# Kernel tuning notes

Hardware: AMD Instinct MI355X
Metric: run time of the kernel (lower is better)

The kernel has to match this reference:

```python
import jax, jax.numpy as jnp
import numpy as np

A_MAX = 7  # 2**A_bits - 1 with A_bits=3
W_HI = 7   # torch.randint(0, 2**W_bits - 1) -> values in [0, 6]


def _conv_valid(x, w):
    # x: [N,C,H,W] float32, w: [O,I,kh,kw] float32; stride 1, no padding
    return jax.lax.conv_general_dilated(
        x, w, window_strides=(1, 1), padding='VALID',
        dimension_numbers=('NCHW', 'OIHW', 'NCHW'))


def setup_inputs() -> dict:
    key = jax.random.key(0)
    k_x, k_w = jax.random.split(key)
    x = jax.random.randint(k_x, (16, 64, 112, 112), 0, 8, dtype=jnp.int32)
    # 3-bit weights of the original 7x7 conv, values 0..6
    W7 = jax.random.randint(k_w, (128, 64, 7, 7), 0, W_HI).astype(jnp.float32)
    w1 = W7[:, :, :, 0:3]
    w2 = W7[:, :, :, 2:5]
    w2 = w2.at[:, :, :, 0].set(0.0)
    w2 = w2.at[:, :, :, 2].set(0.0)
    w3 = W7[:, :, :, 4:7]
    return {"x": x, "w1": w1, "w2": w2, "w3": w3}


def reference(x, w1, w2, w3):
    # 3-bit activation quantization: clip int input to [0, 7]
    xc = jnp.clip(x, 0, A_MAX).astype(jnp.float32)
    out1 = _conv_valid(xc[:, :, :, :-2], w1)   # [N,O,H-6,W-4]
    out2 = _conv_valid(xc, w2)                 # [N,O,H-6,W-2]
    out3 = _conv_valid(xc[:, :, :, 2:], w3)    # [N,O,H-6,W-4]
    # combine slices -> equivalent to valid 7x7 conv: [N,O,H-6,W-6]
    return out1[:, :, :, :-2] + out2[:, :, :, 2:-2] + out3[:, :, :, 2:]
```

## Files before the change

kernel.cpp:

```cpp
#include <hip/hip_runtime.h>
#include <cstdint>

typedef __attribute__((ext_vector_type(4))) int i32x4;

#define XROWS  22
#define ROWB   2048
#define WSLICE 8192
#define WB_BYTES 409600
#define XT_BYTES ((size_t)16 * 112 * 128 * 64)

__device__ __forceinline__ void g2lds16(const void* g, void* l) {
  __builtin_amdgcn_global_load_lds(
      (const __attribute__((address_space(1))) unsigned int*)g,
      (__attribute__((address_space(3))) unsigned int*)l, 16, 0, 0);
}

__global__ void prep_w(const float* __restrict__ w1,
                       const float* __restrict__ w2,
                       const float* __restrict__ w3,
                       signed char* __restrict__ wb) {
  int t = blockIdx.x * 256 + threadIdx.x;
  int lo = t & 15;
  int co = (t >> 4) & 127;
  int g  = (t >> 11) & 3;
  int s  = t >> 13;
  if (s >= 49) return;
  int kh = s / 7, kw = s % 7;
  int ci = g * 16 + lo;
  int base = ((co * 64 + ci) * 7 + kh) * 3;
  float v;
  if (kw < 3)       v = w1[base + kw];
  else if (kw == 3) v = w2[base + 1];
  else              v = w3[base + kw - 4];
  wb[t] = (signed char)(int)v;
}

__global__ void prep_x(const int* __restrict__ x, signed char* __restrict__ xt) {
  __shared__ unsigned char T[64 * 68];
  const int tid = threadIdx.x;
  const int wt = blockIdx.x * 64, h = blockIdx.y, n = blockIdx.z;
  {
    const int wr = tid & 63;
    const int cb = (tid >> 6) * 16;
    int ws = wt + wr; ws = ws < 112 ? ws : 111;
    const int* xp = x + (((size_t)n * 64 + cb) * 112 + h) * 112 + ws;
    #pragma unroll
    for (int g4 = 0; g4 < 4; ++g4) {
      uint32_t v = 0;
      #pragma unroll
      for (int j = 0; j < 4; ++j) {
        int a = xp[(g4 * 4 + j) * 12544];
        a = a < 0 ? 0 : (a > 7 ? 7 : a);
        v |= (uint32_t)a << (8 * j);
      }
      *(uint32_t*)&T[wr * 68 + cb + g4 * 4] = v;
    }
  }
  __syncthreads();
  {
    const int wo = tid >> 2, q = tid & 3;
    const int key = ((wt + wo) >> 1) & 3;
    const int sg = (q ^ key) << 4;
    int4 v;
    v.x = *(const int*)&T[wo * 68 + sg + 0];
    v.y = *(const int*)&T[wo * 68 + sg + 4];
    v.z = *(const int*)&T[wo * 68 + sg + 8];
    v.w = *(const int*)&T[wo * 68 + sg + 12];
    *(int4*)&xt[(((size_t)n * 112 + h) * 128 + wt + wo) * 64 + q * 16] = v;
  }
}

#define MFMA(acc, a, b) acc = __builtin_amdgcn_mfma_i32_16x16x64_i8(a, b, acc, 0, 0, 0)

template<bool XT>
__global__ __launch_bounds__(256, 3)
void conv7(const int* __restrict__ x, const signed char* __restrict__ xt,
           const signed char* __restrict__ wb, float* __restrict__ out) {
  __shared__ __align__(16) unsigned char Xs[XROWS * ROWB];

  const int tid  = threadIdx.x;
  const int lane = tid & 63;
  const int wid  = tid >> 6;
  const int lrow = lane & 15;
  const int lkg  = lane >> 4;

  const int L  = blockIdx.x;
  const int Lp = (L & 7) * 196 + (L >> 3);
  const int coh = Lp & 1;
  const int r2  = Lp >> 1;
  const int bx  = r2 % 7;
  const int t7  = r2 / 7;
  const int by  = t7 % 7;
  const int n   = t7 / 7;
  const int ho_base = by * 16;
  const int wo_base = bx * 16;

  const signed char* aB = wb + lkg * 2048 + coh * 1024 + lrow * 16;

  i32x4 A[4];
  #pragma unroll
  for (int m = 0; m < 4; ++m) A[m] = *(const i32x4*)(aB + m * 256);

  if constexpr (XT) {
    for (int r = wid; r < XROWS; r += 4) {
      int h = ho_base + r; h = h < 112 ? h : 111;
      const signed char* src = xt + (((size_t)n * 112 + h) * 128 + wo_base) * 64;
      g2lds16(src + lane * 16, &Xs[r * ROWB]);
      g2lds16(src + 1024 + lane * 16, &Xs[r * ROWB + 1024]);
    }
    asm volatile("s_waitcnt vmcnt(0)" ::: "memory");
  } else {
    const int w_a  = tid & 15,       cg_a  = tid >> 4;
    const int w_b2 = 16 + (tid & 7), cg_b2 = tid >> 3;
    const bool doB = (tid < 128) && ((tid & 7) < 6);
    const int keyA = ((w_a >> 1) & 3) << 2;
    const int keyB = ((w_b2 >> 1) & 3) << 2;
    for (int r = 0; r < XROWS; ++r) {
      int h = ho_base + r; h = h < 112 ? h : 111;
      const int* xr = x + (size_t)n * 64 * 12544 + h * 112;
      {
        int wc = wo_base + w_a; wc = wc < 112 ? wc : 111;
        uint32_t v = 0;
        #pragma unroll
        for (int j = 0; j < 4; ++j) {
          int a = xr[(cg_a * 4 + j) * 12544 + wc];
          a = a < 0 ? 0 : (a > 7 ? 7 : a);
          v |= (uint32_t)a << (8 * j);
        }
        *(uint32_t*)&Xs[r * ROWB + w_a * 64 + ((cg_a ^ keyA) << 2)] = v;
      }
      if (doB) {
        int wc = wo_base + w_b2; wc = wc < 112 ? wc : 111;
        uint32_t v = 0;
        #pragma unroll
        for (int j = 0; j < 4; ++j) {
          int a = xr[(cg_b2 * 4 + j) * 12544 + wc];
          a = a < 0 ? 0 : (a > 7 ? 7 : a);
          v |= (uint32_t)a << (8 * j);
        }
        *(uint32_t*)&Xs[r * ROWB + w_b2 * 64 + ((cg_b2 ^ keyB) << 2)] = v;
      }
    }
  }
  __syncthreads();

  i32x4 acc[4][4];
  #pragma unroll
  for (int m = 0; m < 4; ++m)
    #pragma unroll
    for (int b = 0; b < 4; ++b)
      acc[m][b] = (i32x4){0, 0, 0, 0};

  const int rowB = wid * 4;

  for (int kw = 0; kw < 7; ++kw) {
    const int w_l  = lrow + kw;
    const int bcol = w_l * 64 + ((lkg ^ ((w_l >> 1) & 3)) << 4);
    i32x4 B[8];
    #pragma unroll
    for (int b = 0; b < 4; ++b)
      B[b] = *(const i32x4*)&Xs[(rowB + b) * ROWB + bcol];

    #pragma unroll
    for (int kh = 0; kh < 7; ++kh) {
      if (kh < 6)
        B[(kh + 4) & 7] = *(const i32x4*)&Xs[(rowB + kh + 4) * ROWB + bcol];
      const signed char* apn = aB + (size_t)(kh < 6 ? (kh + 1) * 7 + kw : kw + 1) * WSLICE;
      __builtin_amdgcn_s_setprio(1);
      #pragma unroll
      for (int m = 0; m < 4; ++m) {
        #pragma unroll
        for (int b = 0; b < 4; ++b)
          MFMA(acc[m][b], A[m], B[(kh + b) & 7]);
        A[m] = *(const i32x4*)(apn + m * 256);
      }
      __builtin_amdgcn_s_setprio(0);
    }
  }

  const int wo = wo_base + lrow;
  if (wo < 106) {
    #pragma unroll
    for (int m = 0; m < 4; ++m) {
      const int co = coh * 64 + m * 16 + lkg * 4;
      #pragma unroll
      for (int b = 0; b < 4; ++b) {
        const int ho = ho_base + rowB + b;
        if (ho < 106) {
          float* op = out + (((size_t)n * 128 + co) * 106 + ho) * 106 + wo;
          #pragma unroll
          for (int j = 0; j < 4; ++j)
            op[(size_t)j * 11236] = (float)acc[m][b][j];
        }
      }
    }
  }
}

extern "C" void kernel_launch(void* const* d_in, const int* in_sizes, int n_in,
                              void* d_out, int out_size, void* d_ws, size_t ws_size,
                              hipStream_t stream) {
  const int*   x  = (const int*)d_in[0];
  const float* w1 = (const float*)d_in[1];
  const float* w2 = (const float*)d_in[2];
  const float* w3 = (const float*)d_in[3];
  float* outp = (float*)d_out;
  signed char* wbp = (signed char*)d_ws;
  signed char* xtp = wbp + WB_BYTES;

  prep_w<<<dim3(1568), dim3(256), 0, stream>>>(w1, w2, w3, wbp);
  if (ws_size >= WB_BYTES + XT_BYTES) {
    prep_x<<<dim3(2, 112, 16), dim3(256), 0, stream>>>(x, xtp);
    conv7<true><<<dim3(1568), dim3(256), 0, stream>>>(x, xtp, wbp, outp);
  } else {
    conv7<false><<<dim3(1568), dim3(256), 0, stream>>>(x, xtp, wbp, outp);
  }
}
```

Before: 84.38 us.

## Fuse weight prep into x prep and make conv a persistent atomic-queue kernel

Merges the weight-packing kernel into the activation-transpose kernel, which saves one launch and also resets a tile counter in workspace. The main conv becomes persistent: 768 blocks pull tiles from a global atomic counter in a loop instead of launching 1568 one-shot blocks. The goals are lower launch overhead and a better-balanced tail. The cost is an atomic plus a barrier per tile, and losing the L2-friendly XCD-aware tile remapping the old kernel used. The setprio hints are also dropped in the fallback path.

```diff
diff --git a/kernel.cpp b/kernel.cpp
--- a/kernel.cpp
+++ b/kernel.cpp
@@ -7,7 +7,10 @@
 #define ROWB   2048
 #define WSLICE 8192
 #define WB_BYTES 409600
+#define CTR_OFF  401408
 #define XT_BYTES ((size_t)16 * 112 * 128 * 64)
+#define NTILES 1568
+#define PERSIST_BLOCKS 768
 
 __device__ __forceinline__ void g2lds16(const void* g, void* l) {
   __builtin_amdgcn_global_load_lds(
@@ -35,10 +38,36 @@
   wb[t] = (signed char)(int)v;
 }
 
-__global__ void prep_x(const int* __restrict__ x, signed char* __restrict__ xt) {
+__global__ void prep_xw(const int* __restrict__ x,
+                        const float* __restrict__ w1,
+                        const float* __restrict__ w2,
+                        const float* __restrict__ w3,
+                        signed char* __restrict__ xt,
+                        signed char* __restrict__ wb,
+                        unsigned int* __restrict__ ctr) {
   __shared__ unsigned char T[64 * 68];
   const int tid = threadIdx.x;
   const int wt = blockIdx.x * 64, h = blockIdx.y, n = blockIdx.z;
+  const int fid = (blockIdx.z * 112 + blockIdx.y) * 2 + blockIdx.x;
+
+  if (fid == 0 && tid == 0) *ctr = 0;
+
+  if (fid < 1568) {
+    int t = fid * 256 + tid;
+    int lo = t & 15;
+    int co = (t >> 4) & 127;
+    int g  = (t >> 11) & 3;
+    int s  = t >> 13;
+    int kh = s / 7, kw = s % 7;
+    int ci = g * 16 + lo;
+    int base = ((co * 64 + ci) * 7 + kh) * 3;
+    float v;
+    if (kw < 3)       v = w1[base + kw];
+    else if (kw == 3) v = w2[base + 1];
+    else              v = w3[base + kw - 4];
+    wb[t] = (signed char)(int)v;
+  }
+
   {
     const int wr = tid & 63;
     const int cb = (tid >> 6) * 16;
@@ -72,10 +101,105 @@
 
 #define MFMA(acc, a, b) acc = __builtin_amdgcn_mfma_i32_16x16x64_i8(a, b, acc, 0, 0, 0)
 
-template<bool XT>
 __global__ __launch_bounds__(256, 3)
-void conv7(const int* __restrict__ x, const signed char* __restrict__ xt,
-           const signed char* __restrict__ wb, float* __restrict__ out) {
+void conv7p(const signed char* __restrict__ xt,
+            const signed char* __restrict__ wb,
+            float* __restrict__ out,
+            unsigned int* __restrict__ ctr) {
+  __shared__ __align__(16) unsigned char Xs[XROWS * ROWB];
+  __shared__ unsigned int ts;
+
+  const int tid  = threadIdx.x;
+  const int lane = tid & 63;
+  const int wid  = tid >> 6;
+  const int lrow = lane & 15;
+  const int lkg  = lane >> 4;
+  const int rowB = wid * 4;
+
+  for (;;) {
+    if (tid == 0) ts = atomicAdd(ctr, 1u);
+    __syncthreads();
+    const unsigned int t = ts;
+    if (t >= NTILES) break;
+
+    const int coh = t & 1;
+    const int r2  = t >> 1;
+    const int bx  = r2 % 7;
+    const int t7  = r2 / 7;
+    const int by  = t7 % 7;
+    const int n   = t7 / 7;
+    const int ho_base = by * 16;
+    const int wo_base = bx * 16;
+
+    const signed char* aB = wb + lkg * 2048 + coh * 1024 + lrow * 16;
+    i32x4 A[4];
+    #pragma unroll
+    for (int m = 0; m < 4; ++m) A[m] = *(const i32x4*)(aB + m * 256);
+
+    for (int r = wid; r < XROWS; r += 4) {
+      int h = ho_base + r; h = h < 112 ? h : 111;
+      const signed char* src = xt + (((size_t)n * 112 + h) * 128 + wo_base) * 64;
+      g2lds16(src + lane * 16, &Xs[r * ROWB]);
+      g2lds16(src + 1024 + lane * 16, &Xs[r * ROWB + 1024]);
+    }
+    asm volatile("s_waitcnt vmcnt(0)" ::: "memory");
+    __syncthreads();
+
+    i32x4 acc[4][4];
+    #pragma unroll
+    for (int m = 0; m < 4; ++m)
+      #pragma unroll
+      for (int b = 0; b < 4; ++b)
+        acc[m][b] = (i32x4){0, 0, 0, 0};
+
+    for (int kw = 0; kw < 7; ++kw) {
+      const int w_l  = lrow + kw;
+      const int bcol = w_l * 64 + ((lkg ^ ((w_l >> 1) & 3)) << 4);
+      i32x4 B[8];
+      #pragma unroll
+      for (int b = 0; b < 4; ++b)
+        B[b] = *(const i32x4*)&Xs[(rowB + b) * ROWB + bcol];
+
+      #pragma unroll
+      for (int kh = 0; kh < 7; ++kh) {
+        if (kh < 6)
+          B[(kh + 4) & 7] = *(const i32x4*)&Xs[(rowB + kh + 4) * ROWB + bcol];
+        const signed char* apn = aB + (size_t)(kh < 6 ? (kh + 1) * 7 + kw : kw + 1) * WSLICE;
+        __builtin_amdgcn_s_setprio(1);
+        #pragma unroll
+        for (int m = 0; m < 4; ++m) {
+          #pragma unroll
+          for (int b = 0; b < 4; ++b)
+            MFMA(acc[m][b], A[m], B[(kh + b) & 7]);
+          A[m] = *(const i32x4*)(apn + m * 256);
+        }
+        __builtin_amdgcn_s_setprio(0);
+      }
+    }
+
+    const int wo = wo_base + lrow;
+    if (wo < 106) {
+      #pragma unroll
+      for (int m = 0; m < 4; ++m) {
+        const int co = coh * 64 + m * 16 + lkg * 4;
+        #pragma unroll
+        for (int b = 0; b < 4; ++b) {
+          const int ho = ho_base + rowB + b;
+          if (ho < 106) {
+            float* op = out + (((size_t)n * 128 + co) * 106 + ho) * 106 + wo;
+            #pragma unroll
+            for (int j = 0; j < 4; ++j)
+              op[(size_t)j * 11236] = (float)acc[m][b][j];
+          }
+        }
+      }
+    }
+  }
+}
+
+__global__ __launch_bounds__(256, 3)
+void conv7f(const int* __restrict__ x,
+            const signed char* __restrict__ wb, float* __restrict__ out) {
   __shared__ __align__(16) unsigned char Xs[XROWS * ROWB];
 
   const int tid  = threadIdx.x;
@@ -96,20 +220,11 @@
   const int wo_base = bx * 16;
 
   const signed char* aB = wb + lkg * 2048 + coh * 1024 + lrow * 16;
-
   i32x4 A[4];
   #pragma unroll
   for (int m = 0; m < 4; ++m) A[m] = *(const i32x4*)(aB + m * 256);
 
-  if constexpr (XT) {
-    for (int r = wid; r < XROWS; r += 4) {
-      int h = ho_base + r; h = h < 112 ? h : 111;
-      const signed char* src = xt + (((size_t)n * 112 + h) * 128 + wo_base) * 64;
-      g2lds16(src + lane * 16, &Xs[r * ROWB]);
-      g2lds16(src + 1024 + lane * 16, &Xs[r * ROWB + 1024]);
-    }
-    asm volatile("s_waitcnt vmcnt(0)" ::: "memory");
-  } else {
+  {
     const int w_a  = tid & 15,       cg_a  = tid >> 4;
     const int w_b2 = 16 + (tid & 7), cg_b2 = tid >> 3;
     const bool doB = (tid < 128) && ((tid & 7) < 6);
@@ -160,13 +275,11 @@
     #pragma unroll
     for (int b = 0; b < 4; ++b)
       B[b] = *(const i32x4*)&Xs[(rowB + b) * ROWB + bcol];
-
     #pragma unroll
     for (int kh = 0; kh < 7; ++kh) {
       if (kh < 6)
         B[(kh + 4) & 7] = *(const i32x4*)&Xs[(rowB + kh + 4) * ROWB + bcol];
       const signed char* apn = aB + (size_t)(kh < 6 ? (kh + 1) * 7 + kw : kw + 1) * WSLICE;
-      __builtin_amdgcn_s_setprio(1);
       #pragma unroll
       for (int m = 0; m < 4; ++m) {
         #pragma unroll
@@ -174,7 +287,6 @@
           MFMA(acc[m][b], A[m], B[(kh + b) & 7]);
         A[m] = *(const i32x4*)(apn + m * 256);
       }
-      __builtin_amdgcn_s_setprio(0);
     }
   }
 
@@ -207,12 +319,13 @@
   float* outp = (float*)d_out;
   signed char* wbp = (signed char*)d_ws;
   signed char* xtp = wbp + WB_BYTES;
-
-  prep_w<<<dim3(1568), dim3(256), 0, stream>>>(w1, w2, w3, wbp);
+  unsigned int* ctr = (unsigned int*)(wbp + CTR_OFF);
+
   if (ws_size >= WB_BYTES + XT_BYTES) {
-    prep_x<<<dim3(2, 112, 16), dim3(256), 0, stream>>>(x, xtp);
-    conv7<true><<<dim3(1568), dim3(256), 0, stream>>>(x, xtp, wbp, outp);
+    prep_xw<<<dim3(2, 112, 16), dim3(256), 0, stream>>>(x, w1, w2, w3, xtp, wbp, ctr);
+    conv7p<<<dim3(PERSIST_BLOCKS), dim3(256), 0, stream>>>(xtp, wbp, outp, ctr);
   } else {
-    conv7<false><<<dim3(1568), dim3(256), 0, stream>>>(x, xtp, wbp, outp);
-  }
-}
+    prep_w<<<dim3(1568), dim3(256), 0, stream>>>(w1, w2, w3, wbp);
+    conv7f<<<dim3(1568), dim3(256), 0, stream>>>(x, wbp, outp);
+  }
+}
```

New measurement: 93.20 us. 10.4% more time.
